# Optimization experiments

Measured on AMD Instinct MI355X. Metric: run time of the kernel, lower is better.

Reference implementation:

```python
import jax, jax.numpy as jnp
import numpy as np

B, S, D, N = 4, 2048, 2048, 4
STREAM = N * D  # 8192


def rmsnorm_apply(x):
    # RMSNorm.apply: eps=1e-6, no learned weight, clamp to [-10, 10]
    xf = x.astype(jnp.float32)
    rms = jnp.sqrt(jnp.mean(xf * xf, axis=-1, keepdims=True) + 1e-6)
    return jnp.clip(xf / rms, -10.0, 10.0).astype(x.dtype)


def sinkhorn_knopp(M, num_iter=20, eps=1e-6):
    # M: (..., n, n) -> doubly-stochastic projection
    M_pos = jnp.exp(jnp.clip(M, -20.0, 20.0))

    def body(_, Mp):
        Mp = Mp / (jnp.sum(Mp, axis=-1, keepdims=True) + eps)
        Mp = Mp / (jnp.sum(Mp, axis=-2, keepdims=True) + eps)
        return Mp

    return jax.lax.fori_loop(0, num_iter, body, M_pos)


def setup_inputs() -> dict:
    key = jax.random.key(0)
    ks = jax.random.split(key, 4)
    std = 0.02
    return {
        "x": jax.random.normal(ks[0], (B, S, STREAM), dtype=jnp.float32),
        "phi_pre": std * jax.random.normal(ks[1], (STREAM, N), dtype=jnp.float32),
        "phi_post": std * jax.random.normal(ks[2], (STREAM, N), dtype=jnp.float32),
        "phi_res": std * jax.random.normal(ks[3], (STREAM, N * N), dtype=jnp.float32),
        "alpha_pre": jnp.float32(0.01),
        "alpha_post": jnp.float32(0.01),
        "alpha_res": jnp.float32(0.01),
        "b_pre": jnp.zeros((1, N), dtype=jnp.float32),
        "b_post": jnp.zeros((1, N), dtype=jnp.float32),
        "b_res": jnp.zeros((N, N), dtype=jnp.float32),
    }


def reference(x, phi_pre, phi_post, phi_res, alpha_pre, alpha_post, alpha_res,
              b_pre, b_post, b_res):
    x_norm = rmsnorm_apply(x)  # (B, S, nC)
    H_pre_t = alpha_pre * (x_norm @ phi_pre) + b_pre            # (B, S, n)
    H_post_t = alpha_post * (x_norm @ phi_post) + b_post        # (B, S, n)
    H_res_t = alpha_res * (x_norm @ phi_res)                    # (B, S, n*n)
    H_res_t = H_res_t.reshape(*H_res_t.shape[:-1], N, N) + b_res
    H_pre = jax.nn.sigmoid(H_pre_t)
    H_post = 2.0 * jax.nn.sigmoid(H_post_t)
    H_res = sinkhorn_knopp(H_res_t, num_iter=20)
    return (H_pre, H_post, H_res)
```

## Files before the change

kernel.cpp:

```cpp
#include <hip/hip_runtime.h>
#include <math.h>

typedef __attribute__((ext_vector_type(8))) short bf16x8;
typedef __attribute__((ext_vector_type(4))) float f32x4;

namespace {
constexpr int D_     = 8192;
constexpr int NROWS  = 8192;
constexpr int RPB    = 16;
constexpr int T      = 512;
constexpr int WAVES  = 8;
constexpr int KSTEPS = D_ / 32;
constexpr int SPW    = KSTEPS / WAVES;
constexpr int OFF_POST = NROWS * 4;
constexpr int OFF_RES  = NROWS * 8;
constexpr size_t WS_NEED = (size_t)KSTEPS * 2 * 64 * 16;

__device__ __forceinline__ short f2bf(float f) {
    union { float f; unsigned u; } c; c.f = f;
    unsigned u = c.u + 0x7fffu + ((c.u >> 16) & 1u);
    return (short)(u >> 16);
}
}

__global__ void prep_bfrag(const float* __restrict__ pre,
                           const float* __restrict__ post,
                           const float* __restrict__ res,
                           uint4* __restrict__ ws)
{
    const int gid  = (int)blockIdx.x * 256 + (int)threadIdx.x;
    const int lane = gid & 63;
    const int n    = (gid >> 6) & 1;
    const int s    = gid >> 7;
    const int g    = lane >> 4;
    const int col  = n * 16 + (lane & 15);
    const int kb   = s * 32 + g * 8;
    unsigned short sv[8];
#pragma unroll
    for (int j = 0; j < 8; ++j) {
        const int k = kb + j;
        float v;
        if      (col < 4)  v = pre [(size_t)k * 4  + col];
        else if (col < 8)  v = post[(size_t)k * 4  + (col - 4)];
        else if (col < 24) v = res [(size_t)k * 16 + (col - 8)];
        else               v = 0.f;
        sv[j] = (unsigned short)f2bf(v);
    }
    uint4 o;
    o.x = (unsigned)sv[0] | ((unsigned)sv[1] << 16);
    o.y = (unsigned)sv[2] | ((unsigned)sv[3] << 16);
    o.z = (unsigned)sv[4] | ((unsigned)sv[5] << 16);
    o.w = (unsigned)sv[6] | ((unsigned)sv[7] << 16);
    ws[((size_t)s * 2 + n) * 64 + lane] = o;
}

template<bool USE_WS>
__global__ __launch_bounds__(T, 4)
void mhc_mfma(const float* __restrict__ x,
              const float* __restrict__ phi_pre,
              const float* __restrict__ phi_post,
              const float* __restrict__ phi_res,
              const float* __restrict__ alpha_pre_p,
              const float* __restrict__ alpha_post_p,
              const float* __restrict__ alpha_res_p,
              const float* __restrict__ b_pre,
              const float* __restrict__ b_post,
              const float* __restrict__ b_res,
              const uint4* __restrict__ bws,
              float* __restrict__ out)
{
    __shared__ float sacc[WAVES][16][32];
    __shared__ float sssq[WAVES][16];
    __shared__ float smxq[WAVES][16];

    const int tid  = (int)threadIdx.x;
    const int wave = tid >> 6;
    const int lane = tid & 63;
    const int arow = lane & 15;
    const int g    = lane >> 4;
    const int row_base = (int)blockIdx.x * RPB;
    const float* __restrict__ xp = x + (size_t)(row_base + arow) * D_ + g * 8;

    f32x4 acc0 = {0.f, 0.f, 0.f, 0.f};
    f32x4 acc1 = {0.f, 0.f, 0.f, 0.f};
    float ssq = 0.f, mxq = 0.f;
    const int s0 = wave * SPW;

#pragma unroll 2
    for (int s = 0; s < SPW; ++s) {
        const int gs = s0 + s;
        const int k0 = gs * 32;
        const float4 a0 = *(const float4*)(xp + k0);
        const float4 a1 = *(const float4*)(xp + k0 + 4);

        bf16x8 bf0, bf1;
        if constexpr (USE_WS) {
            const uint4 b0 = bws[((size_t)gs * 2 + 0) * 64 + lane];
            const uint4 b1 = bws[((size_t)gs * 2 + 1) * 64 + lane];
            __builtin_memcpy(&bf0, &b0, 16);
            __builtin_memcpy(&bf1, &b1, 16);
        } else {
            const int colc = lane & 15;
#pragma unroll
            for (int n = 0; n < 2; ++n) {
                const int col = n * 16 + colc;
                unsigned short sv[8];
#pragma unroll
                for (int j = 0; j < 8; ++j) {
                    const int k = k0 + g * 8 + j;
                    float v;
                    if      (col < 4)  v = phi_pre [(size_t)k * 4  + col];
                    else if (col < 8)  v = phi_post[(size_t)k * 4  + (col - 4)];
                    else if (col < 24) v = phi_res [(size_t)k * 16 + (col - 8)];
                    else               v = 0.f;
                    sv[j] = (unsigned short)f2bf(v);
                }
                uint4 o;
                o.x = (unsigned)sv[0] | ((unsigned)sv[1] << 16);
                o.y = (unsigned)sv[2] | ((unsigned)sv[3] << 16);
                o.z = (unsigned)sv[4] | ((unsigned)sv[5] << 16);
                o.w = (unsigned)sv[6] | ((unsigned)sv[7] << 16);
                if (n == 0) __builtin_memcpy(&bf0, &o, 16);
                else        __builtin_memcpy(&bf1, &o, 16);
            }
        }

        ssq = fmaf(a0.x, a0.x, ssq); ssq = fmaf(a0.y, a0.y, ssq);
        ssq = fmaf(a0.z, a0.z, ssq); ssq = fmaf(a0.w, a0.w, ssq);
        ssq = fmaf(a1.x, a1.x, ssq); ssq = fmaf(a1.y, a1.y, ssq);
        ssq = fmaf(a1.z, a1.z, ssq); ssq = fmaf(a1.w, a1.w, ssq);
        mxq = fmaxf(mxq, fmaxf(fmaxf(a0.x*a0.x, a0.y*a0.y), fmaxf(a0.z*a0.z, a0.w*a0.w)));
        mxq = fmaxf(mxq, fmaxf(fmaxf(a1.x*a1.x, a1.y*a1.y), fmaxf(a1.z*a1.z, a1.w*a1.w)));

        bf16x8 af;
        af[0] = f2bf(a0.x); af[1] = f2bf(a0.y); af[2] = f2bf(a0.z); af[3] = f2bf(a0.w);
        af[4] = f2bf(a1.x); af[5] = f2bf(a1.y); af[6] = f2bf(a1.z); af[7] = f2bf(a1.w);

        acc0 = __builtin_amdgcn_mfma_f32_16x16x32_bf16(af, bf0, acc0, 0, 0, 0);
        acc1 = __builtin_amdgcn_mfma_f32_16x16x32_bf16(af, bf1, acc1, 0, 0, 0);
    }

    ssq += __shfl_xor(ssq, 16); ssq += __shfl_xor(ssq, 32);
    mxq = fmaxf(mxq, __shfl_xor(mxq, 16)); mxq = fmaxf(mxq, __shfl_xor(mxq, 32));

#pragma unroll
    for (int r = 0; r < 4; ++r) {
        sacc[wave][g * 4 + r][arow]      = acc0[r];
        sacc[wave][g * 4 + r][16 + arow] = acc1[r];
    }
    if (lane < 16) { sssq[wave][arow] = ssq; smxq[wave][arow] = mxq; }
    __syncthreads();

    const int erow = tid >> 5;
    const int el   = tid & 31;
    const int orow = row_base + erow;

    float redv = 0.f;
    if (el < 24) {
#pragma unroll
        for (int w = 0; w < WAVES; ++w) redv += sacc[w][erow][el];
    } else if (el == 24) {
#pragma unroll
        for (int w = 0; w < WAVES; ++w) redv += sssq[w][erow];
    }
    float mxrow = smxq[0][erow];
#pragma unroll
    for (int w = 1; w < WAVES; ++w) mxrow = fmaxf(mxrow, smxq[w][erow]);

    const float ssq_tot = __shfl(redv, 24, 32);
    const float msq  = ssq_tot * (1.f / 8192.f) + 1e-6f;
    const float rinv = 1.f / sqrtf(msq);

    const float a_pre  = alpha_pre_p[0];
    const float a_post = alpha_post_p[0];
    const float a_res  = alpha_res_p[0];

    const bool needclamp = (mxrow > 100.f * msq);

    if (!needclamp) {
        const int e = el & 15;
        float m = __shfl(redv, 8 + e, 32);
        m = a_res * m * rinv + b_res[e];
        m = fminf(fmaxf(m, -20.f), 20.f);
        m = expf(m);
        for (int it = 0; it < 20; ++it) {
            float rs = m + __shfl_xor(m, 1);
            rs += __shfl_xor(rs, 2);
            m = m / (rs + 1e-6f);
            float cs = m + __shfl_xor(m, 4);
            cs += __shfl_xor(cs, 8);
            m = m / (cs + 1e-6f);
        }
        if (el < 16)
            out[OFF_RES + (size_t)orow * 16 + el] = m;
        if (el < 4) {
            const float h = a_pre * redv * rinv + b_pre[el];
            out[(size_t)orow * 4 + el] = 1.f / (1.f + expf(-h));
        } else if (el < 8) {
            const float h = a_post * redv * rinv + b_post[el - 4];
            out[OFF_POST + (size_t)orow * 4 + (el - 4)] = 2.f / (1.f + expf(-h));
        }
    } else if (el == 0) {
        const float* __restrict__ xrow = x + (size_t)orow * D_;
        float dp[4] = {0.f,0.f,0.f,0.f}, dq[4] = {0.f,0.f,0.f,0.f};
        float dr[16] = {0.f,0.f,0.f,0.f,0.f,0.f,0.f,0.f,
                        0.f,0.f,0.f,0.f,0.f,0.f,0.f,0.f};
        for (int k = 0; k < D_; ++k) {
            float v = xrow[k] * rinv;
            v = fminf(fmaxf(v, -10.f), 10.f);
            const float4 pp = *(const float4*)(phi_pre  + (size_t)k * 4);
            const float4 pq = *(const float4*)(phi_post + (size_t)k * 4);
            dp[0] = fmaf(v, pp.x, dp[0]); dp[1] = fmaf(v, pp.y, dp[1]);
            dp[2] = fmaf(v, pp.z, dp[2]); dp[3] = fmaf(v, pp.w, dp[3]);
            dq[0] = fmaf(v, pq.x, dq[0]); dq[1] = fmaf(v, pq.y, dq[1]);
            dq[2] = fmaf(v, pq.z, dq[2]); dq[3] = fmaf(v, pq.w, dq[3]);
#pragma unroll
            for (int j2 = 0; j2 < 4; ++j2) {
                const float4 pr = *(const float4*)(phi_res + (size_t)k * 16 + 4 * j2);
                dr[4*j2+0] = fmaf(v, pr.x, dr[4*j2+0]);
                dr[4*j2+1] = fmaf(v, pr.y, dr[4*j2+1]);
                dr[4*j2+2] = fmaf(v, pr.z, dr[4*j2+2]);
                dr[4*j2+3] = fmaf(v, pr.w, dr[4*j2+3]);
            }
        }
        float mm[16];
#pragma unroll
        for (int e2 = 0; e2 < 16; ++e2) {
            float m = a_res * dr[e2] + b_res[e2];
            m = fminf(fmaxf(m, -20.f), 20.f);
            mm[e2] = expf(m);
        }
        for (int it = 0; it < 20; ++it) {
#pragma unroll
            for (int i2 = 0; i2 < 4; ++i2) {
                const float rs = mm[i2*4] + mm[i2*4+1] + mm[i2*4+2] + mm[i2*4+3] + 1e-6f;
#pragma unroll
                for (int j2 = 0; j2 < 4; ++j2) mm[i2*4+j2] /= rs;
            }
#pragma unroll
            for (int j2 = 0; j2 < 4; ++j2) {
                const float cs = mm[j2] + mm[4+j2] + mm[8+j2] + mm[12+j2] + 1e-6f;
#pragma unroll
                for (int i2 = 0; i2 < 4; ++i2) mm[i2*4+j2] /= cs;
            }
        }
#pragma unroll
        for (int j = 0; j < 4; ++j) {
            out[(size_t)orow * 4 + j]            = 1.f / (1.f + expf(-(a_pre  * dp[j] + b_pre[j])));
            out[OFF_POST + (size_t)orow * 4 + j] = 2.f / (1.f + expf(-(a_post * dq[j] + b_post[j])));
        }
#pragma unroll
        for (int e2 = 0; e2 < 16; ++e2)
            out[OFF_RES + (size_t)orow * 16 + e2] = mm[e2];
    }
}

extern "C" void kernel_launch(void* const* d_in, const int* in_sizes, int n_in,
                              void* d_out, int out_size, void* d_ws, size_t ws_size,
                              hipStream_t stream)
{
    const float* x        = (const float*)d_in[0];
    const float* phi_pre  = (const float*)d_in[1];
    const float* phi_post = (const float*)d_in[2];
    const float* phi_res  = (const float*)d_in[3];
    const float* a_pre    = (const float*)d_in[4];
    const float* a_post   = (const float*)d_in[5];
    const float* a_res    = (const float*)d_in[6];
    const float* b_pre    = (const float*)d_in[7];
    const float* b_post   = (const float*)d_in[8];
    const float* b_res    = (const float*)d_in[9];
    float* out = (float*)d_out;

    const bool use_ws = (ws_size >= WS_NEED) && (d_ws != nullptr);
    dim3 grid(NROWS / RPB);
    dim3 block(T);

    if (use_ws) {
        uint4* ws = (uint4*)d_ws;
        hipLaunchKernelGGL(prep_bfrag, dim3(KSTEPS * 2 * 64 / 256), dim3(256), 0, stream,
                           phi_pre, phi_post, phi_res, ws);
        hipLaunchKernelGGL((mhc_mfma<true>), grid, block, 0, stream,
                           x, phi_pre, phi_post, phi_res,
                           a_pre, a_post, a_res, b_pre, b_post, b_res,
                           (const uint4*)ws, out);
    } else {
        hipLaunchKernelGGL((mhc_mfma<false>), grid, block, 0, stream,
                           x, phi_pre, phi_post, phi_res,
                           a_pre, a_post, a_res, b_pre, b_post, b_res,
                           (const uint4*)nullptr, out);
    }
}
```

Baseline: 59.30 us.

## Stream x through swizzled triple-buffered LDS with direct global-to-LDS loads

Rewrites the main kernel so each block loads x chunks of 256 columns into a three-deep LDS ring with global_load_lds, using an XOR swizzle and explicit vmcnt waits plus barriers. Each wave now works on an interleaved k-slice of every chunk instead of a contiguous k-range, and prefetches the next B fragments from the workspace one iteration ahead. The aim is to overlap HBM streaming of x with the MFMA and norm work and to coalesce loads better. In exchange it adds a barrier per chunk, and the LDS ring is reused as the reduction buffer.

```diff
diff --git a/kernel.cpp b/kernel.cpp
--- a/kernel.cpp
+++ b/kernel.cpp
@@ -10,8 +10,10 @@
 constexpr int RPB    = 16;
 constexpr int T      = 512;
 constexpr int WAVES  = 8;
+constexpr int CK     = 256;
+constexpr int NCH    = D_ / CK;
+constexpr int NBUF   = 3;
 constexpr int KSTEPS = D_ / 32;
-constexpr int SPW    = KSTEPS / WAVES;
 constexpr int OFF_POST = NROWS * 4;
 constexpr int OFF_RES  = NROWS * 8;
 constexpr size_t WS_NEED = (size_t)KSTEPS * 2 * 64 * 16;
@@ -20,6 +22,12 @@
     union { float f; unsigned u; } c; c.f = f;
     unsigned u = c.u + 0x7fffu + ((c.u >> 16) & 1u);
     return (short)(u >> 16);
+}
+
+typedef const __attribute__((address_space(1))) void* gas_t;
+typedef __attribute__((address_space(3))) void* las_t;
+__device__ __forceinline__ void ldg_lds16(const void* g, void* l) {
+    __builtin_amdgcn_global_load_lds((gas_t)g, (las_t)l, 16, 0, 0);
 }
 }
 
@@ -54,24 +62,25 @@
     ws[((size_t)s * 2 + n) * 64 + lane] = o;
 }
 
-template<bool USE_WS>
 __global__ __launch_bounds__(T, 4)
-void mhc_mfma(const float* __restrict__ x,
-              const float* __restrict__ phi_pre,
-              const float* __restrict__ phi_post,
-              const float* __restrict__ phi_res,
-              const float* __restrict__ alpha_pre_p,
-              const float* __restrict__ alpha_post_p,
-              const float* __restrict__ alpha_res_p,
-              const float* __restrict__ b_pre,
-              const float* __restrict__ b_post,
-              const float* __restrict__ b_res,
-              const uint4* __restrict__ bws,
-              float* __restrict__ out)
+void mhc_lds(const float* __restrict__ x,
+             const float* __restrict__ phi_pre,
+             const float* __restrict__ phi_post,
+             const float* __restrict__ phi_res,
+             const float* __restrict__ alpha_pre_p,
+             const float* __restrict__ alpha_post_p,
+             const float* __restrict__ alpha_res_p,
+             const float* __restrict__ b_pre,
+             const float* __restrict__ b_post,
+             const float* __restrict__ b_res,
+             const uint4* __restrict__ bws,
+             float* __restrict__ out)
 {
-    __shared__ float sacc[WAVES][16][32];
+    __shared__ __align__(16) char smem[NBUF * RPB * CK * 4];
     __shared__ float sssq[WAVES][16];
     __shared__ float smxq[WAVES][16];
+    float (*xs)[RPB][CK] = (float (*)[RPB][CK])smem;
+    float (*sacc)[16][32] = (float (*)[16][32])smem;
 
     const int tid  = (int)threadIdx.x;
     const int wave = tid >> 6;
@@ -79,66 +88,68 @@
     const int arow = lane & 15;
     const int g    = lane >> 4;
     const int row_base = (int)blockIdx.x * RPB;
-    const float* __restrict__ xp = x + (size_t)(row_base + arow) * D_ + g * 8;
+
+    const int r0 = wave * 2, r1 = r0 + 1;
+    const char* gx0 = (const char*)(x + (size_t)(row_base + r0) * D_);
+    const char* gx1 = (const char*)(x + (size_t)(row_base + r1) * D_);
+    const int lo0 = (lane * 16) ^ ((r0 & 7) << 4);
+    const int lo1 = (lane * 16) ^ ((r1 & 7) << 4);
+
+    ldg_lds16(gx0 + 0 * CK * 4 + lo0, &xs[0][r0][0]);
+    ldg_lds16(gx1 + 0 * CK * 4 + lo1, &xs[0][r1][0]);
+    asm volatile("" ::: "memory");
+    ldg_lds16(gx0 + 1 * CK * 4 + lo0, &xs[1][r0][0]);
+    ldg_lds16(gx1 + 1 * CK * 4 + lo1, &xs[1][r1][0]);
+    asm volatile("" ::: "memory");
+    uint4 bq0 = bws[((size_t)wave * 2 + 0) * 64 + lane];
+    uint4 bq1 = bws[((size_t)wave * 2 + 1) * 64 + lane];
 
     f32x4 acc0 = {0.f, 0.f, 0.f, 0.f};
     f32x4 acc1 = {0.f, 0.f, 0.f, 0.f};
     float ssq = 0.f, mxq = 0.f;
-    const int s0 = wave * SPW;
-
-#pragma unroll 2
-    for (int s = 0; s < SPW; ++s) {
-        const int gs = s0 + s;
-        const int k0 = gs * 32;
-        const float4 a0 = *(const float4*)(xp + k0);
-        const float4 a1 = *(const float4*)(xp + k0 + 4);
-
-        bf16x8 bf0, bf1;
-        if constexpr (USE_WS) {
-            const uint4 b0 = bws[((size_t)gs * 2 + 0) * 64 + lane];
-            const uint4 b1 = bws[((size_t)gs * 2 + 1) * 64 + lane];
-            __builtin_memcpy(&bf0, &b0, 16);
-            __builtin_memcpy(&bf1, &b1, 16);
-        } else {
-            const int colc = lane & 15;
-#pragma unroll
-            for (int n = 0; n < 2; ++n) {
-                const int col = n * 16 + colc;
-                unsigned short sv[8];
-#pragma unroll
-                for (int j = 0; j < 8; ++j) {
-                    const int k = k0 + g * 8 + j;
-                    float v;
-                    if      (col < 4)  v = phi_pre [(size_t)k * 4  + col];
-                    else if (col < 8)  v = phi_post[(size_t)k * 4  + (col - 4)];
-                    else if (col < 24) v = phi_res [(size_t)k * 16 + (col - 8)];
-                    else               v = 0.f;
-                    sv[j] = (unsigned short)f2bf(v);
-                }
-                uint4 o;
-                o.x = (unsigned)sv[0] | ((unsigned)sv[1] << 16);
-                o.y = (unsigned)sv[2] | ((unsigned)sv[3] << 16);
-                o.z = (unsigned)sv[4] | ((unsigned)sv[5] << 16);
-                o.w = (unsigned)sv[6] | ((unsigned)sv[7] << 16);
-                if (n == 0) __builtin_memcpy(&bf0, &o, 16);
-                else        __builtin_memcpy(&bf1, &o, 16);
-            }
-        }
-
-        ssq = fmaf(a0.x, a0.x, ssq); ssq = fmaf(a0.y, a0.y, ssq);
-        ssq = fmaf(a0.z, a0.z, ssq); ssq = fmaf(a0.w, a0.w, ssq);
-        ssq = fmaf(a1.x, a1.x, ssq); ssq = fmaf(a1.y, a1.y, ssq);
-        ssq = fmaf(a1.z, a1.z, ssq); ssq = fmaf(a1.w, a1.w, ssq);
-        mxq = fmaxf(mxq, fmaxf(fmaxf(a0.x*a0.x, a0.y*a0.y), fmaxf(a0.z*a0.z, a0.w*a0.w)));
-        mxq = fmaxf(mxq, fmaxf(fmaxf(a1.x*a1.x, a1.y*a1.y), fmaxf(a1.z*a1.z, a1.w*a1.w)));
-
-        bf16x8 af;
-        af[0] = f2bf(a0.x); af[1] = f2bf(a0.y); af[2] = f2bf(a0.z); af[3] = f2bf(a0.w);
-        af[4] = f2bf(a1.x); af[5] = f2bf(a1.y); af[6] = f2bf(a1.z); af[7] = f2bf(a1.w);
+    const int sw = (arow & 7) << 4;
+    const int b0 = wave * 128 + g * 32;
+
+    for (int c = 0; c < NCH; ++c) {
+        asm volatile("s_waitcnt vmcnt(4)" ::: "memory");
+        __builtin_amdgcn_s_barrier();
+        __builtin_amdgcn_sched_barrier(0);
+
+        const int gn = ((c + 1) & (NCH - 1)) * 8 + wave;
+        const uint4 nb0 = bws[((size_t)gn * 2 + 0) * 64 + lane];
+        const uint4 nb1 = bws[((size_t)gn * 2 + 1) * 64 + lane];
+        asm volatile("" ::: "memory");
+
+        const int cn = (c + 2) & (NCH - 1);
+        const int bn = (c + 2) % NBUF;
+        ldg_lds16(gx0 + (size_t)cn * CK * 4 + lo0, &xs[bn][r0][0]);
+        ldg_lds16(gx1 + (size_t)cn * CK * 4 + lo1, &xs[bn][r1][0]);
+
+        const char* rb = (const char*)&xs[c % NBUF][arow][0];
+        const float4 xa = *(const float4*)(rb + ( b0       ^ sw));
+        const float4 xb = *(const float4*)(rb + ((b0 + 16) ^ sw));
+
+        ssq = fmaf(xa.x, xa.x, ssq); ssq = fmaf(xa.y, xa.y, ssq);
+        ssq = fmaf(xa.z, xa.z, ssq); ssq = fmaf(xa.w, xa.w, ssq);
+        ssq = fmaf(xb.x, xb.x, ssq); ssq = fmaf(xb.y, xb.y, ssq);
+        ssq = fmaf(xb.z, xb.z, ssq); ssq = fmaf(xb.w, xb.w, ssq);
+        mxq = fmaxf(mxq, fmaxf(fmaxf(xa.x*xa.x, xa.y*xa.y), fmaxf(xa.z*xa.z, xa.w*xa.w)));
+        mxq = fmaxf(mxq, fmaxf(fmaxf(xb.x*xb.x, xb.y*xb.y), fmaxf(xb.z*xb.z, xb.w*xb.w)));
+
+        bf16x8 af, bf0, bf1;
+        af[0] = f2bf(xa.x); af[1] = f2bf(xa.y); af[2] = f2bf(xa.z); af[3] = f2bf(xa.w);
+        af[4] = f2bf(xb.x); af[5] = f2bf(xb.y); af[6] = f2bf(xb.z); af[7] = f2bf(xb.w);
+        __builtin_memcpy(&bf0, &bq0, 16);
+        __builtin_memcpy(&bf1, &bq1, 16);
 
         acc0 = __builtin_amdgcn_mfma_f32_16x16x32_bf16(af, bf0, acc0, 0, 0, 0);
         acc1 = __builtin_amdgcn_mfma_f32_16x16x32_bf16(af, bf1, acc1, 0, 0, 0);
-    }
+
+        bq0 = nb0; bq1 = nb1;
+    }
+
+    asm volatile("s_waitcnt vmcnt(0)" ::: "memory");
+    __syncthreads();
 
     ssq += __shfl_xor(ssq, 16); ssq += __shfl_xor(ssq, 32);
     mxq = fmaxf(mxq, __shfl_xor(mxq, 16)); mxq = fmaxf(mxq, __shfl_xor(mxq, 32));
@@ -193,6 +204,187 @@
         }
         if (el < 16)
             out[OFF_RES + (size_t)orow * 16 + el] = m;
+        if (el < 4) {
+            const float h = a_pre * redv * rinv + b_pre[el];
+            out[(size_t)orow * 4 + el] = 1.f / (1.f + expf(-h));
+        } else if (el < 8) {
+            const float h = a_post * redv * rinv + b_post[el - 4];
+            out[OFF_POST + (size_t)orow * 4 + (el - 4)] = 2.f / (1.f + expf(-h));
+        }
+    } else if (el == 0) {
+        const float* __restrict__ xrow = x + (size_t)orow * D_;
+        float dp[4] = {0.f,0.f,0.f,0.f}, dq[4] = {0.f,0.f,0.f,0.f};
+        float dr[16] = {0.f,0.f,0.f,0.f,0.f,0.f,0.f,0.f,
+                        0.f,0.f,0.f,0.f,0.f,0.f,0.f,0.f};
+        for (int k = 0; k < D_; ++k) {
+            float v = xrow[k] * rinv;
+            v = fminf(fmaxf(v, -10.f), 10.f);
+            const float4 pp = *(const float4*)(phi_pre  + (size_t)k * 4);
+            const float4 pq = *(const float4*)(phi_post + (size_t)k * 4);
+            dp[0] = fmaf(v, pp.x, dp[0]); dp[1] = fmaf(v, pp.y, dp[1]);
+            dp[2] = fmaf(v, pp.z, dp[2]); dp[3] = fmaf(v, pp.w, dp[3]);
+            dq[0] = fmaf(v, pq.x, dq[0]); dq[1] = fmaf(v, pq.y, dq[1]);
+            dq[2] = fmaf(v, pq.z, dq[2]); dq[3] = fmaf(v, pq.w, dq[3]);
+#pragma unroll
+            for (int j2 = 0; j2 < 4; ++j2) {
+                const float4 pr = *(const float4*)(phi_res + (size_t)k * 16 + 4 * j2);
+                dr[4*j2+0] = fmaf(v, pr.x, dr[4*j2+0]);
+                dr[4*j2+1] = fmaf(v, pr.y, dr[4*j2+1]);
+                dr[4*j2+2] = fmaf(v, pr.z, dr[4*j2+2]);
+                dr[4*j2+3] = fmaf(v, pr.w, dr[4*j2+3]);
+            }
+        }
+        float mm[16];
+#pragma unroll
+        for (int e2 = 0; e2 < 16; ++e2) {
+            float m = a_res * dr[e2] + b_res[e2];
+            m = fminf(fmaxf(m, -20.f), 20.f);
+            mm[e2] = expf(m);
+        }
+        for (int it = 0; it < 20; ++it) {
+#pragma unroll
+            for (int i2 = 0; i2 < 4; ++i2) {
+                const float rs = mm[i2*4] + mm[i2*4+1] + mm[i2*4+2] + mm[i2*4+3] + 1e-6f;
+#pragma unroll
+                for (int j2 = 0; j2 < 4; ++j2) mm[i2*4+j2] /= rs;
+            }
+#pragma unroll
+            for (int j2 = 0; j2 < 4; ++j2) {
+                const float cs = mm[j2] + mm[4+j2] + mm[8+j2] + mm[12+j2] + 1e-6f;
+#pragma unroll
+                for (int i2 = 0; i2 < 4; ++i2) mm[i2*4+j2] /= cs;
+            }
+        }
+#pragma unroll
+        for (int j = 0; j < 4; ++j) {
+            out[(size_t)orow * 4 + j]            = 1.f / (1.f + expf(-(a_pre  * dp[j] + b_pre[j])));
+            out[OFF_POST + (size_t)orow * 4 + j] = 2.f / (1.f + expf(-(a_post * dq[j] + b_post[j])));
+        }
+#pragma unroll
+        for (int e2 = 0; e2 < 16; ++e2)
+            out[OFF_RES + (size_t)orow * 16 + e2] = mm[e2];
+    }
+}
+
+__global__ __launch_bounds__(T, 4)
+void mhc_plain(const float* __restrict__ x,
+               const float* __restrict__ phi_pre,
+               const float* __restrict__ phi_post,
+               const float* __restrict__ phi_res,
+               const float* __restrict__ alpha_pre_p,
+               const float* __restrict__ alpha_post_p,
+               const float* __restrict__ alpha_res_p,
+               const float* __restrict__ b_pre,
+               const float* __restrict__ b_post,
+               const float* __restrict__ b_res,
+               float* __restrict__ out)
+{
+    __shared__ float sacc[WAVES][16][32];
+    __shared__ float sssq[WAVES][16];
+    __shared__ float smxq[WAVES][16];
+
+    const int tid  = (int)threadIdx.x;
+    const int wave = tid >> 6;
+    const int lane = tid & 63;
+    const int arow = lane & 15;
+    const int g    = lane >> 4;
+    const int row_base = (int)blockIdx.x * RPB;
+    const float* __restrict__ xp = x + (size_t)(row_base + arow) * D_ + g * 8;
+
+    f32x4 acc0 = {0.f, 0.f, 0.f, 0.f};
+    f32x4 acc1 = {0.f, 0.f, 0.f, 0.f};
+    float ssq = 0.f, mxq = 0.f;
+    const int s0 = wave * (KSTEPS / WAVES);
+
+    for (int s = 0; s < KSTEPS / WAVES; ++s) {
+        const int gs = s0 + s;
+        const int k0 = gs * 32;
+        const float4 a0 = *(const float4*)(xp + k0);
+        const float4 a1 = *(const float4*)(xp + k0 + 4);
+        bf16x8 bf0, bf1;
+        const int colc = lane & 15;
+#pragma unroll
+        for (int n = 0; n < 2; ++n) {
+            const int col = n * 16 + colc;
+            unsigned short sv[8];
+#pragma unroll
+            for (int j = 0; j < 8; ++j) {
+                const int k = k0 + g * 8 + j;
+                float v;
+                if      (col < 4)  v = phi_pre [(size_t)k * 4  + col];
+                else if (col < 8)  v = phi_post[(size_t)k * 4  + (col - 4)];
+                else if (col < 24) v = phi_res [(size_t)k * 16 + (col - 8)];
+                else               v = 0.f;
+                sv[j] = (unsigned short)f2bf(v);
+            }
+            uint4 o;
+            o.x = (unsigned)sv[0] | ((unsigned)sv[1] << 16);
+            o.y = (unsigned)sv[2] | ((unsigned)sv[3] << 16);
+            o.z = (unsigned)sv[4] | ((unsigned)sv[5] << 16);
+            o.w = (unsigned)sv[6] | ((unsigned)sv[7] << 16);
+            if (n == 0) __builtin_memcpy(&bf0, &o, 16);
+            else        __builtin_memcpy(&bf1, &o, 16);
+        }
+        ssq = fmaf(a0.x, a0.x, ssq); ssq = fmaf(a0.y, a0.y, ssq);
+        ssq = fmaf(a0.z, a0.z, ssq); ssq = fmaf(a0.w, a0.w, ssq);
+        ssq = fmaf(a1.x, a1.x, ssq); ssq = fmaf(a1.y, a1.y, ssq);
+        ssq = fmaf(a1.z, a1.z, ssq); ssq = fmaf(a1.w, a1.w, ssq);
+        mxq = fmaxf(mxq, fmaxf(fmaxf(a0.x*a0.x, a0.y*a0.y), fmaxf(a0.z*a0.z, a0.w*a0.w)));
+        mxq = fmaxf(mxq, fmaxf(fmaxf(a1.x*a1.x, a1.y*a1.y), fmaxf(a1.z*a1.z, a1.w*a1.w)));
+        bf16x8 af;
+        af[0] = f2bf(a0.x); af[1] = f2bf(a0.y); af[2] = f2bf(a0.z); af[3] = f2bf(a0.w);
+        af[4] = f2bf(a1.x); af[5] = f2bf(a1.y); af[6] = f2bf(a1.z); af[7] = f2bf(a1.w);
+        acc0 = __builtin_amdgcn_mfma_f32_16x16x32_bf16(af, bf0, acc0, 0, 0, 0);
+        acc1 = __builtin_amdgcn_mfma_f32_16x16x32_bf16(af, bf1, acc1, 0, 0, 0);
+    }
+
+    ssq += __shfl_xor(ssq, 16); ssq += __shfl_xor(ssq, 32);
+    mxq = fmaxf(mxq, __shfl_xor(mxq, 16)); mxq = fmaxf(mxq, __shfl_xor(mxq, 32));
+#pragma unroll
+    for (int r = 0; r < 4; ++r) {
+        sacc[wave][g * 4 + r][arow]      = acc0[r];
+        sacc[wave][g * 4 + r][16 + arow] = acc1[r];
+    }
+    if (lane < 16) { sssq[wave][arow] = ssq; smxq[wave][arow] = mxq; }
+    __syncthreads();
+
+    const int erow = tid >> 5;
+    const int el   = tid & 31;
+    const int orow = row_base + erow;
+    float redv = 0.f;
+    if (el < 24) {
+#pragma unroll
+        for (int w = 0; w < WAVES; ++w) redv += sacc[w][erow][el];
+    } else if (el == 24) {
+#pragma unroll
+        for (int w = 0; w < WAVES; ++w) redv += sssq[w][erow];
+    }
+    float mxrow = smxq[0][erow];
+#pragma unroll
+    for (int w = 1; w < WAVES; ++w) mxrow = fmaxf(mxrow, smxq[w][erow]);
+    const float ssq_tot = __shfl(redv, 24, 32);
+    const float msq  = ssq_tot * (1.f / 8192.f) + 1e-6f;
+    const float rinv = 1.f / sqrtf(msq);
+    const float a_pre  = alpha_pre_p[0];
+    const float a_post = alpha_post_p[0];
+    const float a_res  = alpha_res_p[0];
+    const bool needclamp = (mxrow > 100.f * msq);
+
+    if (!needclamp) {
+        const int e = el & 15;
+        float m = __shfl(redv, 8 + e, 32);
+        m = a_res * m * rinv + b_res[e];
+        m = fminf(fmaxf(m, -20.f), 20.f);
+        m = expf(m);
+        for (int it = 0; it < 20; ++it) {
+            float rs = m + __shfl_xor(m, 1);
+            rs += __shfl_xor(rs, 2);
+            m = m / (rs + 1e-6f);
+            float cs = m + __shfl_xor(m, 4);
+            cs += __shfl_xor(cs, 8);
+            m = m / (cs + 1e-6f);
+        }
+        if (el < 16) out[OFF_RES + (size_t)orow * 16 + el] = m;
         if (el < 4) {
             const float h = a_pre * redv * rinv + b_pre[el];
             out[(size_t)orow * 4 + el] = 1.f / (1.f + expf(-h));
@@ -279,14 +471,13 @@
         uint4* ws = (uint4*)d_ws;
         hipLaunchKernelGGL(prep_bfrag, dim3(KSTEPS * 2 * 64 / 256), dim3(256), 0, stream,
                            phi_pre, phi_post, phi_res, ws);
-        hipLaunchKernelGGL((mhc_mfma<true>), grid, block, 0, stream,
+        hipLaunchKernelGGL(mhc_lds, grid, block, 0, stream,
                            x, phi_pre, phi_post, phi_res,
                            a_pre, a_post, a_res, b_pre, b_post, b_res,
                            (const uint4*)ws, out);
     } else {
-        hipLaunchKernelGGL((mhc_mfma<false>), grid, block, 0, stream,
+        hipLaunchKernelGGL(mhc_plain, grid, block, 0, stream,
                            x, phi_pre, phi_post, phi_res,
-                           a_pre, a_post, a_res, b_pre, b_post, b_res,
-                           (const uint4*)nullptr, out);
-    }
-}
+                           a_pre, a_post, a_res, b_pre, b_post, b_res, out);
+    }
+}
```

Result: slower. 68.87 us (+16.1%).
